# Kernel tuning notes

Measured on AMD Instinct MI355X. Metric: run time of the kernel, lower is better.

Reference implementation:

```python
import jax, jax.numpy as jnp
import numpy as np

N = 8192
IN_DIM = 128
THETA_DIM = 256
OUT_DIM = 64
BN_EPS = 1e-5
LEAKY_SLOPE = 0.01


def setup_inputs() -> dict:
    key = jax.random.key(0)
    ks = jax.random.split(key, 8)
    H = jax.random.normal(ks[0], (N, IN_DIM), dtype=jnp.float32)
    # fixed adjacency passed to __init__; nonnegative so mask=ceil(A*1e-5) is {0,1}
    A = jax.random.uniform(ks[1], (N, N), dtype=jnp.float32)
    bn_gamma = jnp.ones((IN_DIM,), dtype=jnp.float32)
    bn_beta = jnp.zeros((IN_DIM,), dtype=jnp.float32)
    W1 = jax.random.normal(ks[2], (IN_DIM, THETA_DIM), dtype=jnp.float32) / np.sqrt(IN_DIM)
    b1 = jnp.zeros((THETA_DIM,), dtype=jnp.float32)
    Wout = jax.random.normal(ks[3], (IN_DIM, OUT_DIM), dtype=jnp.float32) / np.sqrt(IN_DIM)
    bout = jnp.zeros((OUT_DIM,), dtype=jnp.float32)
    return {"H": H, "A": A, "bn_gamma": bn_gamma, "bn_beta": bn_beta,
            "W1": W1, "b1": b1, "Wout": Wout, "bout": bout}


def reference(H, A, bn_gamma, bn_beta, W1, b1, Wout, bout):
    # BatchNorm1d in training mode: batch stats over the N (node) axis, biased var
    mean = jnp.mean(H, axis=0)
    var = jnp.mean(jnp.square(H - mean), axis=0)
    Hn = (H - mean) * jax.lax.rsqrt(var + BN_EPS) * bn_gamma + bn_beta  # [N, IN_DIM]

    Hx = Hn @ W1 + b1                                    # [N, THETA_DIM]
    scores = jax.nn.sigmoid(Hx @ Hx.T)                   # [N, N]
    mask = jnp.ceil(A * 1e-5)                            # binary mask from fixed A
    n = A.shape[0]
    A1 = jnp.maximum(scores, 0.1) * mask + jnp.eye(n, dtype=H.dtype)  # [N, N]

    # D_hat @ A1 @ D_hat is just symmetric row/col scaling by deg^-0.5
    d = jnp.power(jnp.sum(A1, axis=1), -0.5)             # [N]
    A_hat = A1 * d[:, None] * d[None, :]                 # [N, N]

    out = A_hat @ (Hn @ Wout + bout)                     # [N, OUT_DIM]
    out = jnp.where(out >= 0, out, LEAKY_SLOPE * out)    # LeakyReLU(0.01)
    return out, A1
```

## Files before the change

kernel.cpp:

```cpp
#include <hip/hip_runtime.h>
#include <math.h>

#define NN 8192
#define IN_DIM 128
#define THETA_DIM 256
#define OUT_DIM 64

typedef _Float16 half_t;
typedef _Float16 f16x8 __attribute__((ext_vector_type(8)));
typedef _Float16 f16x4 __attribute__((ext_vector_type(4)));
typedef float f32x4 __attribute__((ext_vector_type(4)));

#define WS_SCALE 0
#define WS_SHIFT 128
#define WS_SUM   256
#define WS_SQ    384
#define WS_ROWSUM 512
#define WS_D     8704
#define WS_HN    16896
#define WS_HX    (WS_HN + NN*IN_DIM)
#define WS_Z     (WS_HX + NN*THETA_DIM)
#define WS_OBUF  (WS_Z + NN*OUT_DIM)
#define WS_ZDHT  (WS_OBUF + NN*OUT_DIM)
#define WS_MASK  (WS_ZDHT + NN*OUT_DIM/2)

__global__ __launch_bounds__(256) void k_zero(float* __restrict__ ws) {
    int b = blockIdx.x, tid = threadIdx.x;
    float4 z = (float4){0.f, 0.f, 0.f, 0.f};
    if (b < 9) {
        int i = b * 256 + tid;
        if (i < 2112) ((float4*)(ws + WS_SUM))[i] = z;
    } else {
        int i = (b - 9) * 256 + tid;
        ((float4*)(ws + WS_OBUF))[i] = z;
    }
}

__global__ __launch_bounds__(256) void k_stats(const float* __restrict__ H, float* __restrict__ ws) {
    int tid = threadIdx.x;
    int c = tid & 127, h = tid >> 7;
    int rb = blockIdx.x * 128;
    float s = 0.f, q = 0.f;
    for (int r = h; r < 128; r += 2) {
        float v = H[(size_t)(rb + r) * IN_DIM + c];
        s += v; q += v * v;
    }
    atomicAdd(&ws[WS_SUM + c], s);
    atomicAdd(&ws[WS_SQ + c], q);
}

__global__ void k_finalize(const float* __restrict__ gamma, const float* __restrict__ beta, float* __restrict__ ws) {
    int c = threadIdx.x;
    float mean = ws[WS_SUM + c] * (1.f / NN);
    float var  = ws[WS_SQ + c] * (1.f / NN) - mean * mean;
    float rstd = 1.f / sqrtf(var + 1e-5f);
    float sc = rstd * gamma[c];
    ws[WS_SCALE + c] = sc;
    ws[WS_SHIFT + c] = beta[c] - mean * sc;
}

__global__ __launch_bounds__(256) void k_hn(const float* __restrict__ H, const float* __restrict__ ws, float* __restrict__ Hn) {
    int i = blockIdx.x * 256 + threadIdx.x;
    const float4* H4 = (const float4*)H;
    float4 v = H4[i];
    int cb = (i & 31) * 4;
    float4 sc = *(const float4*)&ws[WS_SCALE + cb];
    float4 sh = *(const float4*)&ws[WS_SHIFT + cb];
    float4 o;
    o.x = v.x * sc.x + sh.x; o.y = v.y * sc.y + sh.y;
    o.z = v.z * sc.z + sh.z; o.w = v.w * sc.w + sh.w;
    ((float4*)Hn)[i] = o;
}

__global__ __launch_bounds__(256) void k_mask(const float* __restrict__ Amat, unsigned int* __restrict__ mask) {
    int idx = blockIdx.x * 256 + threadIdx.x;
    const float4* A4 = (const float4*)Amat;
#pragma unroll
    for (int it = 0; it < 4; it++) {
        int g = idx + it * 524288;
        unsigned int bits = 0u;
#pragma unroll
        for (int w = 0; w < 8; w++) {
            float4 a = A4[(size_t)g * 8 + w];
            bits |= (a.x > 0.f ? 1u : 0u) << (w * 4 + 0);
            bits |= (a.y > 0.f ? 1u : 0u) << (w * 4 + 1);
            bits |= (a.z > 0.f ? 1u : 0u) << (w * 4 + 2);
            bits |= (a.w > 0.f ? 1u : 0u) << (w * 4 + 3);
        }
        mask[g] = bits;
    }
}

__global__ __launch_bounds__(256) void k_hx(const float* __restrict__ Hn, const float* __restrict__ W1,
                                            const float* __restrict__ b1, half_t* __restrict__ Hx) {
    __shared__ float HnS[32 * IN_DIM];
    int tid = threadIdx.x;
    int row0 = blockIdx.x * 32;
    const float4* src = (const float4*)(Hn + (size_t)row0 * IN_DIM);
    float4* dst = (float4*)HnS;
#pragma unroll
    for (int q = 0; q < 4; q++) dst[q * 256 + tid] = src[q * 256 + tid];
    __syncthreads();
    int c = tid;
    float acc[32];
#pragma unroll
    for (int r = 0; r < 32; r++) acc[r] = 0.f;
    for (int k0 = 0; k0 < IN_DIM; k0 += 4) {
        float w0 = W1[(size_t)(k0 + 0) * THETA_DIM + c];
        float w1 = W1[(size_t)(k0 + 1) * THETA_DIM + c];
        float w2 = W1[(size_t)(k0 + 2) * THETA_DIM + c];
        float w3 = W1[(size_t)(k0 + 3) * THETA_DIM + c];
#pragma unroll
        for (int r = 0; r < 32; r++) {
            float4 h = *(const float4*)&HnS[r * IN_DIM + k0];
            acc[r] += h.x * w0 + h.y * w1 + h.z * w2 + h.w * w3;
        }
    }
    float bb = b1[c];
#pragma unroll
    for (int r = 0; r < 32; r++) Hx[(size_t)(row0 + r) * THETA_DIM + c] = (half_t)(acc[r] + bb);
}

__global__ __launch_bounds__(256) void k_y(const float* __restrict__ Hn, const float* __restrict__ Wout,
                                           const float* __restrict__ bout, float* __restrict__ Y) {
    __shared__ float HnS[64 * IN_DIM];
    int tid = threadIdx.x;
    int row0 = blockIdx.x * 64;
    const float4* src = (const float4*)(Hn + (size_t)row0 * IN_DIM);
    float4* dst = (float4*)HnS;
#pragma unroll
    for (int q = 0; q < 8; q++) dst[q * 256 + tid] = src[q * 256 + tid];
    __syncthreads();
    int c = tid & 63, rg = tid >> 6;
    float acc[16];
#pragma unroll
    for (int r = 0; r < 16; r++) acc[r] = 0.f;
    for (int k0 = 0; k0 < IN_DIM; k0 += 4) {
        float w0 = Wout[(size_t)(k0 + 0) * OUT_DIM + c];
        float w1 = Wout[(size_t)(k0 + 1) * OUT_DIM + c];
        float w2 = Wout[(size_t)(k0 + 2) * OUT_DIM + c];
        float w3 = Wout[(size_t)(k0 + 3) * OUT_DIM + c];
#pragma unroll
        for (int r = 0; r < 16; r++) {
            float4 h = *(const float4*)&HnS[(rg * 16 + r) * IN_DIM + k0];
            acc[r] += h.x * w0 + h.y * w1 + h.z * w2 + h.w * w3;
        }
    }
    float bb = bout[c];
#pragma unroll
    for (int r = 0; r < 16; r++) Y[(size_t)(row0 + rg * 16 + r) * OUT_DIM + c] = acc[r] + bb;
}

__global__ __launch_bounds__(256) void k_scores(const half_t* __restrict__ Hx,
                                                const unsigned char* __restrict__ mask,
                                                float* __restrict__ A1, float* __restrict__ rowsum) {
    __shared__ half_t Rs[128 * 72];
    __shared__ half_t Cs[128 * 72];
    int tid = threadIdx.x;
    int R = blockIdx.x * 128, C = blockIdx.y * 128;
    int lane = tid & 63, wv = tid >> 6;
    int li = lane & 15, lg = lane >> 4;
    int qi = (wv >> 1) * 64, qj = (wv & 1) * 64;
    int su = tid & 7;

    f32x4 acc[4][4];
#pragma unroll
    for (int t = 0; t < 4; t++)
#pragma unroll
        for (int u = 0; u < 4; u++) acc[t][u] = (f32x4){0.f, 0.f, 0.f, 0.f};

    f16x8 ra[4], rb[4];
#pragma unroll
    for (int q = 0; q < 4; q++) {
        int r = (q * 256 + tid) >> 3;
        ra[q] = *(const f16x8*)(Hx + (size_t)(R + r) * THETA_DIM + su * 8);
        rb[q] = *(const f16x8*)(Hx + (size_t)(C + r) * THETA_DIM + su * 8);
    }

    for (int s = 0; s < 4; s++) {
        __syncthreads();
#pragma unroll
        for (int q = 0; q < 4; q++) {
            int r = (q * 256 + tid) >> 3;
            *(f16x8*)(Rs + r * 72 + su * 8) = ra[q];
            *(f16x8*)(Cs + r * 72 + su * 8) = rb[q];
        }
        if (s < 3) {
            int k0 = (s + 1) * 64;
#pragma unroll
            for (int q = 0; q < 4; q++) {
                int r = (q * 256 + tid) >> 3;
                ra[q] = *(const f16x8*)(Hx + (size_t)(R + r) * THETA_DIM + k0 + su * 8);
                rb[q] = *(const f16x8*)(Hx + (size_t)(C + r) * THETA_DIM + k0 + su * 8);
            }
        }
        __syncthreads();
#pragma unroll
        for (int kk = 0; kk < 2; kk++) {
            f16x8 af[4], bf[4];
#pragma unroll
            for (int t = 0; t < 4; t++)
                af[t] = *(const f16x8*)(Cs + (qi + t * 16 + li) * 72 + kk * 32 + lg * 8);
#pragma unroll
            for (int u = 0; u < 4; u++)
                bf[u] = *(const f16x8*)(Rs + (qj + u * 16 + li) * 72 + kk * 32 + lg * 8);
#pragma unroll
            for (int t = 0; t < 4; t++)
#pragma unroll
                for (int u = 0; u < 4; u++)
                    acc[t][u] = __builtin_amdgcn_mfma_f32_16x16x32_f16(af[t], bf[u], acc[t][u], 0, 0, 0);
        }
    }

#pragma unroll
    for (int u = 0; u < 4; u++) {
        int gr = R + qj + u * 16 + li;
        unsigned long long m64 = *(const unsigned long long*)&mask[(size_t)gr * 1024 + ((C + qi) >> 3)];
        float rsum = 0.f;
#pragma unroll
        for (int t = 0; t < 4; t++) {
            int gc0 = C + qi + t * 16 + lg * 4;
            float4 wv4;
            float* pv = (float*)&wv4;
#pragma unroll
            for (int jj = 0; jj < 4; jj++) {
                float x = acc[t][u][jj];
                float sg = 1.f / (1.f + __expf(-x));
                float m = (float)((m64 >> (t * 16 + lg * 4 + jj)) & 1ULL);
                float v = fmaxf(sg, 0.1f) * m + ((gr == gc0 + jj) ? 1.f : 0.f);
                pv[jj] = v;
                rsum += v;
            }
            *(float4*)&A1[(size_t)gr * NN + gc0] = wv4;
        }
        rsum += __shfl_xor(rsum, 16, 64);
        rsum += __shfl_xor(rsum, 32, 64);
        if (lg == 0) atomicAdd(&rowsum[gr], rsum);
    }
}

__global__ void k_dvec(float* __restrict__ ws) {
    int i = blockIdx.x * 256 + threadIdx.x;
    ws[WS_D + i] = 1.f / sqrtf(ws[WS_ROWSUM + i]);
}

__global__ __launch_bounds__(256) void k_scalez(const float* __restrict__ dvec, const float* __restrict__ Z,
                                                half_t* __restrict__ ZdhT) {
    __shared__ float T[64 * 68];
    int tid = threadIdx.x;
    int j0 = blockIdx.x * 64;
#pragma unroll
    for (int q = 0; q < 4; q++) {
        int unit = q * 256 + tid;
        int j = unit >> 4, c4 = (unit & 15) * 4;
        float dj = dvec[j0 + j];
        float4 v = *(const float4*)&Z[(size_t)(j0 + j) * OUT_DIM + c4];
        v.x *= dj; v.y *= dj; v.z *= dj; v.w *= dj;
        *(float4*)&T[j * 68 + c4] = v;
    }
    __syncthreads();
#pragma unroll
    for (int q = 0; q < 2; q++) {
        int unit = q * 256 + tid;
        int c = unit >> 3, j8 = (unit & 7) * 8;
        f16x8 h;
#pragma unroll
        for (int x = 0; x < 8; x++) h[x] = (half_t)T[(j8 + x) * 68 + c];
        *(f16x8*)&ZdhT[(size_t)c * NN + j0 + j8] = h;
    }
}

__global__ __launch_bounds__(256) void k_spmm(const float* __restrict__ A1, const half_t* __restrict__ ZdhT,
                                              float* __restrict__ obuf) {
    __shared__ half_t As[128 * 72];
    __shared__ half_t Bs[64 * 72];
    int tid = threadIdx.x;
    int row0 = blockIdx.x * 128;
    int j0 = blockIdx.y * 512;
    int lane = tid & 63, wv = tid >> 6;
    int li = lane & 15, lg = lane >> 4;
    int ar = tid >> 4, ac4 = (tid & 15) * 4;
    int bn = tid >> 3, bk8 = (tid & 7) * 8;

    f32x4 acc[2][4];
#pragma unroll
    for (int t = 0; t < 2; t++)
#pragma unroll
        for (int u = 0; u < 4; u++) acc[t][u] = (f32x4){0.f, 0.f, 0.f, 0.f};

    float4 va[8];
    f16x8 vb[2];
#pragma unroll
    for (int q = 0; q < 8; q++)
        va[q] = *(const float4*)&A1[(size_t)(row0 + (q * 16 + ar)) * NN + j0 + ac4];
#pragma unroll
    for (int q = 0; q < 2; q++)
        vb[q] = *(const f16x8*)&ZdhT[(size_t)(q * 32 + bn) * NN + j0 + bk8];

    for (int jc = j0; jc < j0 + 512; jc += 64) {
        __syncthreads();
#pragma unroll
        for (int q = 0; q < 8; q++) {
            f16x4 h; h[0] = (half_t)va[q].x; h[1] = (half_t)va[q].y; h[2] = (half_t)va[q].z; h[3] = (half_t)va[q].w;
            *(f16x4*)&As[(q * 16 + ar) * 72 + ac4] = h;
        }
#pragma unroll
        for (int q = 0; q < 2; q++)
            *(f16x8*)&Bs[(q * 32 + bn) * 72 + bk8] = vb[q];
        if (jc + 64 < j0 + 512) {
#pragma unroll
            for (int q = 0; q < 8; q++)
                va[q] = *(const float4*)&A1[(size_t)(row0 + (q * 16 + ar)) * NN + jc + 64 + ac4];
#pragma unroll
            for (int q = 0; q < 2; q++)
                vb[q] = *(const f16x8*)&ZdhT[(size_t)(q * 32 + bn) * NN + jc + 64 + bk8];
        }
        __syncthreads();
#pragma unroll
        for (int kk = 0; kk < 2; kk++) {
            f16x8 af[2], bf[4];
#pragma unroll
            for (int t = 0; t < 2; t++)
                af[t] = *(const f16x8*)&As[(wv * 32 + t * 16 + li) * 72 + kk * 32 + lg * 8];
#pragma unroll
            for (int u = 0; u < 4; u++)
                bf[u] = *(const f16x8*)&Bs[(u * 16 + li) * 72 + kk * 32 + lg * 8];
#pragma unroll
            for (int t = 0; t < 2; t++)
#pragma unroll
                for (int u = 0; u < 4; u++)
                    acc[t][u] = __builtin_amdgcn_mfma_f32_16x16x32_f16(af[t], bf[u], acc[t][u], 0, 0, 0);
        }
    }
#pragma unroll
    for (int t = 0; t < 2; t++)
#pragma unroll
        for (int u = 0; u < 4; u++)
#pragma unroll
            for (int r = 0; r < 4; r++)
                atomicAdd(&obuf[(size_t)(row0 + wv * 32 + t * 16 + lg * 4 + r) * OUT_DIM + u * 16 + li],
                          acc[t][u][r]);
}

__global__ void k_out(const float* __restrict__ ws, float* __restrict__ out) {
    int i = blockIdx.x * 256 + threadIdx.x;
    const float4* O4 = (const float4*)(ws + WS_OBUF);
    int row = i >> 4;
    float d = ws[WS_D + row];
    float4 v = O4[i];
    float a = d * v.x, b = d * v.y, cc = d * v.z, e = d * v.w;
    v.x = (a >= 0.f) ? a : 0.01f * a;
    v.y = (b >= 0.f) ? b : 0.01f * b;
    v.z = (cc >= 0.f) ? cc : 0.01f * cc;
    v.w = (e >= 0.f) ? e : 0.01f * e;
    ((float4*)out)[i] = v;
}

extern "C" void kernel_launch(void* const* d_in, const int* in_sizes, int n_in,
                              void* d_out, int out_size, void* d_ws, size_t ws_size,
                              hipStream_t stream) {
    const float* H     = (const float*)d_in[0];
    const float* A     = (const float*)d_in[1];
    const float* gamma = (const float*)d_in[2];
    const float* beta  = (const float*)d_in[3];
    const float* W1    = (const float*)d_in[4];
    const float* b1    = (const float*)d_in[5];
    const float* Wout  = (const float*)d_in[6];
    const float* bout  = (const float*)d_in[7];
    float* out = (float*)d_out;
    float* A1  = out + (size_t)NN * OUT_DIM;
    float* ws  = (float*)d_ws;
    half_t* Hx = (half_t*)(ws + WS_HX);
    half_t* ZdhT = (half_t*)(ws + WS_ZDHT);
    unsigned int* maskw = (unsigned int*)(ws + WS_MASK);

    k_zero<<<521, 256, 0, stream>>>(ws);
    k_mask<<<2048, 256, 0, stream>>>(A, maskw);
    k_stats<<<64, 256, 0, stream>>>(H, ws);
    k_finalize<<<1, 128, 0, stream>>>(gamma, beta, ws);
    k_hn<<<1024, 256, 0, stream>>>(H, ws, ws + WS_HN);
    k_hx<<<256, 256, 0, stream>>>(ws + WS_HN, W1, b1, Hx);
    k_y<<<128, 256, 0, stream>>>(ws + WS_HN, Wout, bout, ws + WS_Z);
    dim3 g6(64, 64);
    k_scores<<<g6, 256, 0, stream>>>(Hx, (const unsigned char*)maskw, A1, ws + WS_ROWSUM);
    k_dvec<<<32, 256, 0, stream>>>(ws);
    k_scalez<<<128, 256, 0, stream>>>(ws + WS_D, ws + WS_Z, ZdhT);
    k_spmm<<<dim3(64, 16), 256, 0, stream>>>(A1, ZdhT, ws + WS_OBUF);
    k_out<<<512, 256, 0, stream>>>(ws, out);
}
```

Before: 337.8 us.

## Emit fp16 copy of A1 for SpMM and replace atomics with partial buffers

When the workspace is large enough, the scores kernel also writes a half-precision copy of A1, and the SpMM reads that copy instead of the fp32 output. Per-column-block partial results go to separate buffers, which a final kernel sums before scaling and LeakyReLU. This is meant to halve SpMM read traffic and remove atomic contention. In exchange it adds an extra 128MB write in the scores kernel and partial-buffer traffic, and it falls back to the old path if the workspace is too small.

```diff
diff --git a/kernel.cpp b/kernel.cpp
--- a/kernel.cpp
+++ b/kernel.cpp
@@ -23,6 +23,9 @@
 #define WS_OBUF  (WS_Z + NN*OUT_DIM)
 #define WS_ZDHT  (WS_OBUF + NN*OUT_DIM)
 #define WS_MASK  (WS_ZDHT + NN*OUT_DIM/2)
+#define WS_OBUFP (WS_MASK + NN*(NN/32))
+#define WS_A1H   (WS_OBUFP + 16*NN*OUT_DIM)
+#define WS_TOTAL ((size_t)WS_A1H + (size_t)NN*NN/2)
 
 __global__ __launch_bounds__(256) void k_zero(float* __restrict__ ws) {
     int b = blockIdx.x, tid = threadIdx.x;
@@ -153,7 +156,8 @@
 
 __global__ __launch_bounds__(256) void k_scores(const half_t* __restrict__ Hx,
                                                 const unsigned char* __restrict__ mask,
-                                                float* __restrict__ A1, float* __restrict__ rowsum) {
+                                                float* __restrict__ A1, float* __restrict__ rowsum,
+                                                half_t* __restrict__ A1h) {
     __shared__ half_t Rs[128 * 72];
     __shared__ half_t Cs[128 * 72];
     int tid = threadIdx.x;
@@ -232,6 +236,12 @@
                 rsum += v;
             }
             *(float4*)&A1[(size_t)gr * NN + gc0] = wv4;
+            if (A1h) {
+                f16x4 h4;
+                h4[0] = (half_t)pv[0]; h4[1] = (half_t)pv[1];
+                h4[2] = (half_t)pv[2]; h4[3] = (half_t)pv[3];
+                *(f16x4*)&A1h[(size_t)gr * NN + gc0] = h4;
+            }
         }
         rsum += __shfl_xor(rsum, 16, 64);
         rsum += __shfl_xor(rsum, 32, 64);
@@ -270,8 +280,77 @@
     }
 }
 
-__global__ __launch_bounds__(256) void k_spmm(const float* __restrict__ A1, const half_t* __restrict__ ZdhT,
-                                              float* __restrict__ obuf) {
+__global__ __launch_bounds__(256) void k_spmm_h(const half_t* __restrict__ A1h, const half_t* __restrict__ ZdhT,
+                                                float* __restrict__ obufP) {
+    __shared__ half_t As[128 * 72];
+    __shared__ half_t Bs[64 * 72];
+    int tid = threadIdx.x;
+    int row0 = blockIdx.x * 128;
+    int j0 = blockIdx.y * 512;
+    int lane = tid & 63, wv = tid >> 6;
+    int li = lane & 15, lg = lane >> 4;
+    int ar = tid >> 3, au8 = (tid & 7) * 8;
+    int bn = tid >> 3, bk8 = (tid & 7) * 8;
+
+    f32x4 acc[2][4];
+#pragma unroll
+    for (int t = 0; t < 2; t++)
+#pragma unroll
+        for (int u = 0; u < 4; u++) acc[t][u] = (f32x4){0.f, 0.f, 0.f, 0.f};
+
+    f16x8 va[4], vb[2];
+#pragma unroll
+    for (int q = 0; q < 4; q++)
+        va[q] = *(const f16x8*)&A1h[(size_t)(row0 + q * 32 + ar) * NN + j0 + au8];
+#pragma unroll
+    for (int q = 0; q < 2; q++)
+        vb[q] = *(const f16x8*)&ZdhT[(size_t)(q * 32 + bn) * NN + j0 + bk8];
+
+    for (int jc = j0; jc < j0 + 512; jc += 64) {
+        __syncthreads();
+#pragma unroll
+        for (int q = 0; q < 4; q++)
+            *(f16x8*)&As[(q * 32 + ar) * 72 + au8] = va[q];
+#pragma unroll
+        for (int q = 0; q < 2; q++)
+            *(f16x8*)&Bs[(q * 32 + bn) * 72 + bk8] = vb[q];
+        if (jc + 64 < j0 + 512) {
+#pragma unroll
+            for (int q = 0; q < 4; q++)
+                va[q] = *(const f16x8*)&A1h[(size_t)(row0 + q * 32 + ar) * NN + jc + 64 + au8];
+#pragma unroll
+            for (int q = 0; q < 2; q++)
+                vb[q] = *(const f16x8*)&ZdhT[(size_t)(q * 32 + bn) * NN + jc + 64 + bk8];
+        }
+        __syncthreads();
+#pragma unroll
+        for (int kk = 0; kk < 2; kk++) {
+            f16x8 af[2], bf[4];
+#pragma unroll
+            for (int t = 0; t < 2; t++)
+                af[t] = *(const f16x8*)&As[(wv * 32 + t * 16 + li) * 72 + kk * 32 + lg * 8];
+#pragma unroll
+            for (int u = 0; u < 4; u++)
+                bf[u] = *(const f16x8*)&Bs[(u * 16 + li) * 72 + kk * 32 + lg * 8];
+#pragma unroll
+            for (int t = 0; t < 2; t++)
+#pragma unroll
+                for (int u = 0; u < 4; u++)
+                    acc[t][u] = __builtin_amdgcn_mfma_f32_16x16x32_f16(af[t], bf[u], acc[t][u], 0, 0, 0);
+        }
+    }
+    float* P = obufP + (size_t)blockIdx.y * NN * OUT_DIM;
+#pragma unroll
+    for (int t = 0; t < 2; t++)
+#pragma unroll
+        for (int u = 0; u < 4; u++)
+#pragma unroll
+            for (int r = 0; r < 4; r++)
+                P[(size_t)(row0 + wv * 32 + t * 16 + lg * 4 + r) * OUT_DIM + u * 16 + li] = acc[t][u][r];
+}
+
+__global__ __launch_bounds__(256) void k_spmm_f32(const float* __restrict__ A1, const half_t* __restrict__ ZdhT,
+                                                  float* __restrict__ obuf) {
     __shared__ half_t As[128 * 72];
     __shared__ half_t Bs[64 * 72];
     int tid = threadIdx.x;
@@ -340,6 +419,26 @@
             for (int r = 0; r < 4; r++)
                 atomicAdd(&obuf[(size_t)(row0 + wv * 32 + t * 16 + lg * 4 + r) * OUT_DIM + u * 16 + li],
                           acc[t][u][r]);
+}
+
+__global__ void k_out_p(const float* __restrict__ ws, float* __restrict__ out) {
+    int i = blockIdx.x * 256 + threadIdx.x;
+    const float4* P = (const float4*)(ws + WS_OBUFP);
+    float4 s = P[i];
+#pragma unroll
+    for (int p = 1; p < 16; p++) {
+        float4 v = P[(size_t)p * 131072 + i];
+        s.x += v.x; s.y += v.y; s.z += v.z; s.w += v.w;
+    }
+    int row = i >> 4;
+    float d = ws[WS_D + row];
+    float a = d * s.x, b = d * s.y, cc = d * s.z, e = d * s.w;
+    float4 v;
+    v.x = (a >= 0.f) ? a : 0.01f * a;
+    v.y = (b >= 0.f) ? b : 0.01f * b;
+    v.z = (cc >= 0.f) ? cc : 0.01f * cc;
+    v.w = (e >= 0.f) ? e : 0.01f * e;
+    ((float4*)out)[i] = v;
 }
 
 __global__ void k_out(const float* __restrict__ ws, float* __restrict__ out) {
@@ -373,6 +472,8 @@
     half_t* Hx = (half_t*)(ws + WS_HX);
     half_t* ZdhT = (half_t*)(ws + WS_ZDHT);
     unsigned int* maskw = (unsigned int*)(ws + WS_MASK);
+    half_t* A1h = (half_t*)(ws + WS_A1H);
+    bool big = ws_size >= WS_TOTAL * sizeof(float);
 
     k_zero<<<521, 256, 0, stream>>>(ws);
     k_mask<<<2048, 256, 0, stream>>>(A, maskw);
@@ -382,9 +483,15 @@
     k_hx<<<256, 256, 0, stream>>>(ws + WS_HN, W1, b1, Hx);
     k_y<<<128, 256, 0, stream>>>(ws + WS_HN, Wout, bout, ws + WS_Z);
     dim3 g6(64, 64);
-    k_scores<<<g6, 256, 0, stream>>>(Hx, (const unsigned char*)maskw, A1, ws + WS_ROWSUM);
+    k_scores<<<g6, 256, 0, stream>>>(Hx, (const unsigned char*)maskw, A1, ws + WS_ROWSUM,
+                                     big ? A1h : (half_t*)nullptr);
     k_dvec<<<32, 256, 0, stream>>>(ws);
     k_scalez<<<128, 256, 0, stream>>>(ws + WS_D, ws + WS_Z, ZdhT);
-    k_spmm<<<dim3(64, 16), 256, 0, stream>>>(A1, ZdhT, ws + WS_OBUF);
-    k_out<<<512, 256, 0, stream>>>(ws, out);
-}
+    if (big) {
+        k_spmm_h<<<dim3(64, 16), 256, 0, stream>>>(A1h, ZdhT, ws + WS_OBUFP);
+        k_out_p<<<512, 256, 0, stream>>>(ws, out);
+    } else {
+        k_spmm_f32<<<dim3(64, 16), 256, 0, stream>>>(A1, ZdhT, ws + WS_OBUF);
+        k_out<<<512, 256, 0, stream>>>(ws, out);
+    }
+}
```

Measured after the change: 361.7 us. +7.1%, slower.
